# Performance work log

Hardware: AMD Instinct MI355X
Metric: run time of the kernel (lower is better)

The kernel has to match this reference:

```python
import jax, jax.numpy as jnp
import numpy as np

B, Q, MAXK, C, D, H, NL = 64, 16, 32, 64, 768, 512, 2
S = Q * (MAXK + 1) + 1  # max padded sequence length (529)


def lstm_layer(x, w_ih, w_hh, b_ih, b_hh):
    # x: [B, S, Din]; torch gate order i, f, g, o
    xg = jnp.einsum('bsd,gd->bsg', x, w_ih) + b_ih + b_hh  # [B,S,4H]
    h0 = jnp.zeros((x.shape[0], w_hh.shape[1]), x.dtype)

    def step(carry, xt):
        h, c = carry
        g = xt + h @ w_hh.T
        i, f, gg, o = jnp.split(g, 4, axis=-1)
        c = jax.nn.sigmoid(f) * c + jax.nn.sigmoid(i) * jnp.tanh(gg)
        h = jax.nn.sigmoid(o) * jnp.tanh(c)
        return (h, c), h

    _, hs = jax.lax.scan(step, (h0, h0), jnp.swapaxes(xg, 0, 1))
    return jnp.swapaxes(hs, 0, 1)  # [B,S,H]


def build_sequence(text_output, questions_outputs, code_embedding, num_snapshots, que_num):
    # Vectorized equivalent of the nested scatter loops.
    valid_q = jnp.arange(Q)[None, :] < que_num[:, None]          # [B,Q]
    qlen = jnp.where(valid_q, num_snapshots + 1, 0)              # per-question block length
    starts = jnp.cumsum(qlen, axis=1) - qlen                     # exclusive cumsum: block start
    L = jnp.sum(qlen, axis=1)                                    # text position; seq_len = L+1

    buf = jnp.zeros((B, S + 1, D), text_output.dtype)            # extra dump slot at index S
    b1 = jnp.arange(B)[:, None]

    # scatter question embeddings at block starts
    q_dest = jnp.where(valid_q, starts, S)
    buf = buf.at[b1, q_dest].set(questions_outputs)

    # scatter code snapshots: dest = start+1+k, src = code_embedding[b, i+k] (as in source)
    k = jnp.arange(MAXK)
    ns = jnp.where(valid_q, num_snapshots, 0)
    valid_s = k[None, None, :] < ns[:, :, None]                  # [B,Q,K]
    dest = jnp.where(valid_s, starts[:, :, None] + 1 + k[None, None, :], S)
    src = jnp.clip(jnp.arange(Q)[:, None] + k[None, :], 0, C - 1)  # [Q,K]
    code_vals = code_embedding[:, src]                           # [B,Q,K,D]
    buf = buf.at[jnp.arange(B)[:, None, None], dest].set(code_vals)

    # current-question text embedding at end of sequence
    buf = buf.at[jnp.arange(B), L].set(text_output)
    return buf[:, :S], L


def setup_inputs() -> dict:
    key = jax.random.key(0)
    ks = jax.random.split(key, 16)
    inp = {
        'text_output': jax.random.normal(ks[0], (B, D), jnp.float32),
        'questions_outputs': jax.random.normal(ks[1], (B, Q, D), jnp.float32),
        'code_embedding': jax.random.normal(ks[2], (B, C, D), jnp.float32),
        'num_snapshots': jax.random.randint(ks[3], (B, Q), 1, MAXK + 1, jnp.int32),
        'que_num': jax.random.randint(ks[4], (B,), 1, Q + 1, jnp.int32),
    }
    s = 0.02
    inp['w_ih_l0'] = jax.random.normal(ks[5], (4 * H, D), jnp.float32) * s
    inp['w_hh_l0'] = jax.random.normal(ks[6], (4 * H, H), jnp.float32) * s
    inp['b_ih_l0'] = jnp.zeros((4 * H,), jnp.float32)
    inp['b_hh_l0'] = jnp.zeros((4 * H,), jnp.float32)
    inp['w_ih_l1'] = jax.random.normal(ks[7], (4 * H, H), jnp.float32) * s
    inp['w_hh_l1'] = jax.random.normal(ks[8], (4 * H, H), jnp.float32) * s
    inp['b_ih_l1'] = jnp.zeros((4 * H,), jnp.float32)
    inp['b_hh_l1'] = jnp.zeros((4 * H,), jnp.float32)
    inp['fc_w'] = jax.random.normal(ks[9], (1, H), jnp.float32) * s
    inp['fc_b'] = jnp.zeros((1,), jnp.float32)
    return inp


def reference(text_output, questions_outputs, code_embedding, num_snapshots, que_num,
              w_ih_l0, w_hh_l0, b_ih_l0, b_hh_l0,
              w_ih_l1, w_hh_l1, b_ih_l1, b_hh_l1, fc_w, fc_b):
    x, L = build_sequence(text_output, questions_outputs, code_embedding, num_snapshots, que_num)
    h = lstm_layer(x, w_ih_l0, w_hh_l0, b_ih_l0, b_hh_l0)
    h = lstm_layer(h, w_ih_l1, w_hh_l1, b_ih_l1, b_hh_l1)
    last = h[jnp.arange(B), L]  # output at seq_len-1 (= text position)
    return last @ fc_w.T + fc_b  # [B, 1]
```

## Files before the change

### kernel.cpp

```cpp
#include <hip/hip_runtime.h>
#include <hip/hip_cooperative_groups.h>

namespace cg = cooperative_groups;

#define B_    64
#define Q_    16
#define MAXK_ 32
#define C_    64
#define D_    768
#define H_    512
#define G4_   2048
#define S_    529
#define NR_   81

typedef float f32x4_t __attribute__((ext_vector_type(4)));
typedef unsigned int u32x2_t __attribute__((ext_vector_type(2)));
typedef unsigned int u32x4_t __attribute__((ext_vector_type(4)));
typedef _Float16 f16x8_t __attribute__((ext_vector_type(8)));

static constexpr size_t OFF_L     = 0;
static constexpr size_t OFF_MAXL  = 256;
static constexpr size_t OFF_MAP   = 512;
static constexpr size_t OFF_BIAS0 = OFF_MAP   + 135424;
static constexpr size_t OFF_BIAS1 = OFF_BIAS0 + 8192;
static constexpr size_t OFF_C0    = OFF_BIAS1 + 8192;
static constexpr size_t OFF_C1    = OFF_C0    + 131072;
static constexpr size_t OFF_HLAST = OFF_C1    + 131072;
static constexpr size_t OFF_H0B   = OFF_HLAST + 131072;
static constexpr size_t OFF_H1B   = OFF_H0B   + 262144;
static constexpr size_t OFF_WTIH0 = OFF_H1B   + 262144;
static constexpr size_t OFF_XPROJ = OFF_WTIH0 + 6291456ULL;
static constexpr size_t OFF_BAR   = OFF_XPROJ + 42467328ULL;
static constexpr size_t OFF_ORD   = OFF_BAR   + 4096;
static constexpr size_t OFF_GMAX  = OFF_ORD   + 256;
static constexpr size_t WS_NEED   = OFF_GMAX  + 256;

__device__ __forceinline__ int group_base(int g) {
  return (g == 0) ? 0 : (g == 1) ? 16 : (g == 2) ? 48 : 32;
}

__device__ __forceinline__ void store_us_cc(ushort* p, unsigned int v) {
  asm volatile("global_store_short %0, %1, off sc0 sc1" :: "v"(p), "v"(v) : "memory");
}
__device__ __forceinline__ void store_f_cc(float* p, float v) {
  asm volatile("global_store_dword %0, %1, off sc0 sc1" :: "v"(p), "v"(v) : "memory");
}
__device__ __forceinline__ void load_a_cc(u32x4_t& v, const ushort* p) {
  asm volatile("global_load_dwordx4 %0, %1, off sc0 sc1" : "=v"(v) : "v"(p) : "memory");
}

__device__ __forceinline__ unsigned int pkrtz(float a, float b) {
  auto r = __builtin_amdgcn_cvt_pkrtz(a, b);
  unsigned int u;
  __builtin_memcpy(&u, &r, 4);
  return u;
}
__device__ __forceinline__ unsigned int f2h(float a) {
  return pkrtz(a, 0.f) & 0xffffu;
}
__device__ __forceinline__ f32x4_t mfma16(u32x4_t a, u32x4_t b, f32x4_t c) {
  f16x8_t av, bv;
  __builtin_memcpy(&av, &a, 16);
  __builtin_memcpy(&bv, &b, 16);
  return __builtin_amdgcn_mfma_f32_16x16x32_f16(av, bv, c, 0, 0, 0);
}

__device__ __forceinline__ float sigm(float x) { return 1.f/(1.f + __expf(-x)); }

#define PSEG 1280
#define PCOL 20

__global__ __launch_bounds__(256) void k_prep(
    const int* __restrict__ ns, const int* __restrict__ que,
    const float* __restrict__ b_ih0, const float* __restrict__ b_hh0,
    const float* __restrict__ b_ih1, const float* __restrict__ b_hh1,
    int* __restrict__ Lp, int* __restrict__ maxLp, int* __restrict__ map,
    float* __restrict__ bias0, float* __restrict__ bias1,
    float* __restrict__ c0, float* __restrict__ c1, float* __restrict__ hlast,
    ushort* __restrict__ h0b, ushort* __restrict__ h1b, int* __restrict__ bar,
    int* __restrict__ ord, int* __restrict__ gmax)
{
  const int tid = threadIdx.x;
  for (int i = tid; i < B_*S_; i += 256) map[i] = -1;
  for (int i = tid; i < G4_; i += 256) {
    bias0[i] = b_ih0[i] + b_hh0[i];
    bias1[i] = b_ih1[i] + b_hh1[i];
  }
  int* h0i = (int*)h0b;
  int* h1i = (int*)h1b;
  for (int i = tid; i < B_*H_; i += 256) {
    c0[i]=0.f; c1[i]=0.f; hlast[i]=0.f;
    h0i[i]=0; h1i[i]=0;
  }
  for (int i = tid; i < 1024; i += 256) bar[i] = 0;
  if (tid == 0) *maxLp = 0;
  __syncthreads();
  if (tid < B_) {
    const int b = tid;
    const int qn = que[b];
    int pos = 0;
    int* m = map + b*S_;
    for (int q = 0; q < qn; ++q) {
      m[pos++] = q;
      const int n = ns[b*Q_ + q];
      for (int k = 0; k < n; ++k) {
        int j = q + k; if (j > C_-1) j = C_-1;
        m[pos++] = 16 + j;
      }
    }
    m[pos] = 80;
    Lp[b] = pos;
    atomicMax(maxLp, pos);
  }
  __syncthreads();
  if (tid < B_) {
    const int myL = Lp[tid];
    int rank = 0;
    for (int j = 0; j < B_; ++j) {
      const int lj = Lp[j];
      rank += (lj > myL) || (lj == myL && j < tid);
    }
    ord[rank] = tid;
  }
  __syncthreads();
  if (tid < 4) {
    const int gb = (tid == 0) ? 0 : (tid == 1) ? 16 : (tid == 2) ? 48 : 32;
    gmax[tid] = Lp[ord[gb]];
  }
}

__global__ __launch_bounds__(256) void k_transpose(
    const float* __restrict__ w, float* __restrict__ wT)
{
  __shared__ float tile[32][33];
  const int n0 = blockIdx.x * 32;
  const int k0 = blockIdx.y * 32;
  const int tx = threadIdx.x, ty = threadIdx.y;
  for (int i = ty; i < 32; i += 8)
    tile[i][tx] = w[(size_t)(n0+i)*D_ + k0 + tx];
  __syncthreads();
  for (int i = ty; i < 32; i += 8)
    wT[(size_t)(k0 + i)*G4_ + n0 + tx] = tile[tx][i];
}

__global__ __launch_bounds__(128, 2) void k_proj(
    const float* __restrict__ text, const float* __restrict__ ques,
    const float* __restrict__ code, const float* __restrict__ wT_ih0,
    const float* __restrict__ bias0, float* __restrict__ xproj)
{
  __shared__ float hsLds[32][64];
  const int mb = blockIdx.x, nb = blockIdx.y;
  const int n0 = nb * 128;
  const int tid = threadIdx.x;
  const int tb = tid >> 4, tn = tid & 15;
  const int b0 = tb * 8;
  const int bb = tid >> 1, hh = tid & 1;

  const int mrow = mb*64 + bb;
  const int sb = mrow / NR_, sr = mrow % NR_;
  const float* srcrow = (sr < 16) ? (ques + ((size_t)sb*Q_ + sr)*D_)
                      : (sr < 80) ? (code + ((size_t)sb*C_ + (sr-16))*D_)
                                  : (text + (size_t)sb*D_);

  float a[8][8];
  #pragma unroll
  for (int i=0;i<8;i++)
    #pragma unroll
    for (int j=0;j<8;j++) a[i][j]=0.f;

  for (int k0 = 0; k0 < D_; k0 += 32) {
    __syncthreads();
    {
      const float* p = srcrow + k0 + hh*16;
      float4 v0 = *(const float4*)(p+0);
      float4 v1 = *(const float4*)(p+4);
      float4 v2 = *(const float4*)(p+8);
      float4 v3 = *(const float4*)(p+12);
      const int kk = hh*16;
      hsLds[kk+ 0][bb]=v0.x; hsLds[kk+ 1][bb]=v0.y; hsLds[kk+ 2][bb]=v0.z; hsLds[kk+ 3][bb]=v0.w;
      hsLds[kk+ 4][bb]=v1.x; hsLds[kk+ 5][bb]=v1.y; hsLds[kk+ 6][bb]=v1.z; hsLds[kk+ 7][bb]=v1.w;
      hsLds[kk+ 8][bb]=v2.x; hsLds[kk+ 9][bb]=v2.y; hsLds[kk+10][bb]=v2.z; hsLds[kk+11][bb]=v2.w;
      hsLds[kk+12][bb]=v3.x; hsLds[kk+13][bb]=v3.y; hsLds[kk+14][bb]=v3.z; hsLds[kk+15][bb]=v3.w;
    }
    __syncthreads();
    const float* wb = wT_ih0 + (size_t)k0*G4_ + n0 + tn*8;
    #pragma unroll 4
    for (int k=0;k<32;k++){
      float4 w0 = *(const float4*)(wb + (size_t)k*G4_);
      float4 w1 = *(const float4*)(wb + (size_t)k*G4_ + 4);
      float4 hA = *(const float4*)(&hsLds[k][b0]);
      float4 hB = *(const float4*)(&hsLds[k][b0+4]);
      float hv[8]={hA.x,hA.y,hA.z,hA.w,hB.x,hB.y,hB.z,hB.w};
      float wv[8]={w0.x,w0.y,w0.z,w0.w,w1.x,w1.y,w1.z,w1.w};
      #pragma unroll
      for (int i=0;i<8;i++)
        #pragma unroll
        for (int j=0;j<8;j++)
          a[i][j] = fmaf(hv[i], wv[j], a[i][j]);
    }
  }
  float bz[8];
  #pragma unroll
  for (int j=0;j<8;j++) bz[j] = bias0[n0 + tn*8 + j];
  #pragma unroll
  for (int i=0;i<8;i++){
    const int m = mb*64 + b0 + i;
    float* pd = xproj + (size_t)m*G4_ + n0 + tn*8;
    *(float4*)(pd+0) = make_float4(a[i][0]+bz[0], a[i][1]+bz[1], a[i][2]+bz[2], a[i][3]+bz[3]);
    *(float4*)(pd+4) = make_float4(a[i][4]+bz[4], a[i][5]+bz[5], a[i][6]+bz[6], a[i][7]+bz[7]);
  }
}


__device__ __forceinline__ void load_wfrags(int tid, int us,
    const float* __restrict__ w_hh0, const float* __restrict__ w_ih1,
    const float* __restrict__ w_hh1, u32x4_t* wf0, u32x4_t* wf1)
{
  const int wv = tid >> 6, lane = tid & 63;
  const int nidx = lane & 15, kgrp = lane >> 4;
  #pragma unroll
  for (int nt = 0; nt < 4; ++nt) {
    const int ngl = (nidx >> 2)*H_ + us*16 + nt*4 + (nidx & 3);
    const float* r0 = w_hh0 + (size_t)ngl*H_ + wv*128 + kgrp*8;
    #pragma unroll
    for (int f = 0; f < 4; ++f) {
      float4 lo = *(const float4*)(r0 + f*32);
      float4 hi = *(const float4*)(r0 + f*32 + 4);
      wf0[nt*4+f] = (u32x4_t){pkrtz(lo.x,lo.y), pkrtz(lo.z,lo.w), pkrtz(hi.x,hi.y), pkrtz(hi.z,hi.w)};
    }
    const float* w1 = (wv < 2) ? w_ih1 : w_hh1;
    const float* r1 = w1 + (size_t)ngl*H_ + (wv & 1)*256 + kgrp*8;
    #pragma unroll
    for (int f = 0; f < 8; ++f) {
      float4 lo = *(const float4*)(r1 + f*32);
      float4 hi = *(const float4*)(r1 + f*32 + 4);
      wf1[nt*8+f] = (u32x4_t){pkrtz(lo.x,lo.y), pkrtz(lo.z,lo.w), pkrtz(hi.x,hi.y), pkrtz(hi.z,hi.w)};
    }
  }
}

__device__ __forceinline__ void xg_prefetch(int t, int maxLg,
    const int* __restrict__ mrow, const float* __restrict__ xbase,
    float& xg0, float& xg1, float& xg2, float& xg3, int& rpre)
{
  rpre = (t <= maxLg) ? mrow[t] : -1;
  const float* xp = xbase + (size_t)(rpre < 0 ? 0 : rpre)*G4_;
  xg0 = xp[0]; xg1 = xp[512]; xg2 = xp[1024]; xg3 = xp[1536];
}

__device__ __forceinline__ void lstm_iter(int t, int maxLg, int gbase, int us,
    const u32x4_t* wf0, const u32x4_t* wf1, float* __restrict__ P,
    const ushort* __restrict__ h0c, ushort* __restrict__ h0n,
    const ushort* __restrict__ h1c, ushort* __restrict__ h1n,
    float* __restrict__ c0, float* __restrict__ c1, float* __restrict__ hlast,
    const int* __restrict__ mrow, const float* __restrict__ xbase,
    float& xg0, float& xg1, float& xg2, float& xg3, int& rpre0, int& rpre1,
    float b1v0, float b1v1, float b1v2, float b1v3, int Lrb, int rb)
{
  const int tid = threadIdx.x;
  const int wv = tid >> 6, lane = tid & 63;
  const int nidx = lane & 15, kgrp = lane >> 4;

  u32x4_t a0[4], a1[8];
  {
    const ushort* h0r = h0c + (size_t)(gbase + nidx)*H_ + wv*128 + kgrp*8;
    #pragma unroll
    for (int f = 0; f < 4; ++f) load_a_cc(a0[f], h0r + f*32);
    const ushort* hs1 = (wv < 2) ? h0c : h1c;
    const ushort* h1r = hs1 + (size_t)(gbase + nidx)*H_ + (wv & 1)*256 + kgrp*8;
    #pragma unroll
    for (int f = 0; f < 8; ++f) load_a_cc(a1[f], h1r + f*32);
  }
  asm volatile("s_waitcnt vmcnt(0)" ::: "memory");
  __builtin_amdgcn_sched_barrier(0);

  f32x4_t acc0[4], acc1[4];
  #pragma unroll
  for (int nt = 0; nt < 4; ++nt) { acc0[nt] = (f32x4_t){0.f,0.f,0.f,0.f}; acc1[nt] = (f32x4_t){0.f,0.f,0.f,0.f}; }
  #pragma unroll
  for (int nt = 0; nt < 4; ++nt)
    #pragma unroll
    for (int f = 0; f < 4; ++f) acc0[nt] = mfma16(a0[f], wf0[nt*4+f], acc0[nt]);
  #pragma unroll
  for (int nt = 0; nt < 4; ++nt)
    #pragma unroll
    for (int f = 0; f < 8; ++f) acc1[nt] = mfma16(a1[f], wf1[nt*8+f], acc1[nt]);

  #pragma unroll
  for (int nt = 0; nt < 4; ++nt) {
    *(f32x4_t*)(P + (wv*2+0)*PSEG + (nt*16 + nidx)*PCOL + kgrp*4) = acc0[nt];
    *(f32x4_t*)(P + (wv*2+1)*PSEG + (nt*16 + nidx)*PCOL + kgrp*4) = acc1[nt];
  }

  float nxg0=xg0, nxg1=xg1, nxg2=xg2, nxg3=xg3;
  int nr0 = -1;
  const int nr1 = rpre0;
  xg_prefetch(t + 1, maxLg, mrow, xbase, nxg0, nxg1, nxg2, nxg3, nr0);
  __syncthreads();

  const int bl = tid & 15, ul = tid >> 4;
  const int pb = gbase + bl;
  const int u = us*16 + ul;
  const int idx = pb*H_ + u;
  const int clb = (ul >> 2)*16 + (ul & 3);
  if (rpre0 >= 0) {
    float g0=xg0, g1=xg1, g2=xg2, g3=xg3;
    #pragma unroll
    for (int w = 0; w < 4; ++w) {
      const float* Pr = P + (w*2+0)*PSEG + bl;
      g0 += Pr[(clb+ 0)*PCOL]; g1 += Pr[(clb+ 4)*PCOL];
      g2 += Pr[(clb+ 8)*PCOL]; g3 += Pr[(clb+12)*PCOL];
    }
    const float cc = sigm(g1)*c0[idx] + sigm(g0)*tanhf(g2);
    c0[idx] = cc;
    store_us_cc(h0n + idx, f2h(sigm(g3)*tanhf(cc)));
  }
  if (rpre1 >= 0) {
    float g0=b1v0, g1=b1v1, g2=b1v2, g3=b1v3;
    #pragma unroll
    for (int w = 0; w < 4; ++w) {
      const float* Pr = P + (w*2+1)*PSEG + bl;
      g0 += Pr[(clb+ 0)*PCOL]; g1 += Pr[(clb+ 4)*PCOL];
      g2 += Pr[(clb+ 8)*PCOL]; g3 += Pr[(clb+12)*PCOL];
    }
    const float cc = sigm(g1)*c1[idx] + sigm(g0)*tanhf(g2);
    c1[idx] = cc;
    const float hn = sigm(g3)*tanhf(cc);
    store_us_cc(h1n + idx, f2h(hn));
    if (t - 1 == Lrb) store_f_cc(hlast + rb*H_ + u, hn);
  }

  xg0 = nxg0; xg1 = nxg1; xg2 = nxg2; xg3 = nxg3;
  rpre0 = nr0; rpre1 = nr1;
}

__device__ __forceinline__ void grid_barrier_g(int* __restrict__ cnt, int gen)
{
  asm volatile("s_waitcnt vmcnt(0)" ::: "memory");
  __syncthreads();
  if (threadIdx.x == 0) {
    atomicAdd(cnt, 1);
    while (__hip_atomic_load(cnt, __ATOMIC_RELAXED, __HIP_MEMORY_SCOPE_AGENT) < gen*32)
      __builtin_amdgcn_s_sleep(1);
  }
  __syncthreads();
}

__global__ __launch_bounds__(256, 1) void k_lstm_coop(
    const float* __restrict__ w_hh0, const float* __restrict__ w_ih1,
    const float* __restrict__ w_hh1, const float* __restrict__ xproj,
    const float* __restrict__ bias1, const int* __restrict__ Lp,
    const int* __restrict__ gmax, const int* __restrict__ map,
    const int* __restrict__ ord,
    ushort* __restrict__ h0b, ushort* __restrict__ h1b,
    float* __restrict__ c0, float* __restrict__ c1, float* __restrict__ hlast,
    const float* __restrict__ fcw, const float* __restrict__ fcb,
    float* __restrict__ out, int* __restrict__ bar)
{
  __shared__ __align__(16) float P[8*PSEG];
  const int blk = blockIdx.x;
  const int g = blk >> 5, us = blk & 31;
  const int gbase = group_base(g);
  const int tid = threadIdx.x;

  u32x4_t wf0[16], wf1[32];
  load_wfrags(tid, us, w_hh0, w_ih1, w_hh1, wf0, wf1);
  const int maxLg = gmax[g];
  int* cnt = bar + g*64;

  const int rb = ord[gbase + (tid & 15)];
  const int* mrow = map + rb*S_;
  const int u = us*16 + (tid >> 4);
  const float* xbase = xproj + (size_t)rb*NR_*G4_ + u;
  const float b1v0 = bias1[u], b1v1 = bias1[512+u], b1v2 = bias1[1024+u], b1v3 = bias1[1536+u];
  const int Lrb = Lp[rb];

  float xg0=0.f, xg1=0.f, xg2=0.f, xg3=0.f;
  int rpre0 = -1, rpre1 = -1;
  xg_prefetch(0, maxLg, mrow, xbase, xg0, xg1, xg2, xg3, rpre0);
  __syncthreads();

  for (int t = 0; t <= maxLg + 1; ++t) {
    const ushort* h0c = h0b + (size_t)(t & 1)*(B_*H_);
    ushort*       h0n = h0b + (size_t)((t+1) & 1)*(B_*H_);
    const ushort* h1c = h1b + (size_t)(t & 1)*(B_*H_);
    ushort*       h1n = h1b + (size_t)((t+1) & 1)*(B_*H_);
    lstm_iter(t, maxLg, gbase, us, wf0, wf1, P,
              h0c, h0n, h1c, h1n, c0, c1, hlast,
              mrow, xbase, xg0, xg1, xg2, xg3, rpre0, rpre1,
              b1v0, b1v1, b1v2, b1v3, Lrb, rb);
    grid_barrier_g(cnt, t + 1);
  }
  if (us == 0 && tid < 32) {
    const int pb = gbase + (tid >> 1), half = tid & 1;
    const int rbf = ord[pb];
    const float* hv = hlast + (size_t)rbf*H_ + half*256;
    const float* fw = fcw + half*256;
    float s = 0.f;
    #pragma unroll 8
    for (int uu = 0; uu < 256; ++uu) s = fmaf(hv[uu], fw[uu], s);
    s += __shfl_xor(s, 1);
    if (half == 0) store_f_cc(out + rbf, s + fcb[0]);
  }
}

__global__ __launch_bounds__(256, 1) void k_step(int t,
    const float* __restrict__ w_hh0, const float* __restrict__ w_ih1,
    const float* __restrict__ w_hh1, const float* __restrict__ xproj,
    const float* __restrict__ bias1, const int* __restrict__ Lp,
    const int* __restrict__ gmax, const int* __restrict__ map,
    const int* __restrict__ ord,
    ushort* __restrict__ h0b, ushort* __restrict__ h1b,
    float* __restrict__ c0, float* __restrict__ c1, float* __restrict__ hlast)
{
  __shared__ __align__(16) float P[8*PSEG];
  const int blk = blockIdx.x;
  const int g = blk >> 5, us = blk & 31;
  const int gbase = group_base(g);
  const int maxLg = gmax[g];
  if (t > maxLg + 1) return;
  const int tid = threadIdx.x;
  u32x4_t wf0[16], wf1[32];
  load_wfrags(tid, us, w_hh0, w_ih1, w_hh1, wf0, wf1);

  const int rb = ord[gbase + (tid & 15)];
  const int* mrow = map + rb*S_;
  const int u = us*16 + (tid >> 4);
  const float* xbase = xproj + (size_t)rb*NR_*G4_ + u;
  const float b1v0 = bias1[u], b1v1 = bias1[512+u], b1v2 = bias1[1024+u], b1v3 = bias1[1536+u];
  const int Lrb = Lp[rb];

  float xg0=0.f, xg1=0.f, xg2=0.f, xg3=0.f;
  int rpre0 = -1, rpre1 = -1;
  xg_prefetch(t, maxLg, mrow, xbase, xg0, xg1, xg2, xg3, rpre0);
  rpre1 = (t-1 >= 0 && t-1 <= maxLg) ? mrow[t-1] : -1;
  __syncthreads();

  const ushort* h0c = h0b + (size_t)(t & 1)*(B_*H_);
  ushort*       h0n = h0b + (size_t)((t+1) & 1)*(B_*H_);
  const ushort* h1c = h1b + (size_t)(t & 1)*(B_*H_);
  ushort*       h1n = h1b + (size_t)((t+1) & 1)*(B_*H_);
  lstm_iter(t, maxLg, gbase, us, wf0, wf1, P,
            h0c, h0n, h1c, h1n, c0, c1, hlast,
            mrow, xbase, xg0, xg1, xg2, xg3, rpre0, rpre1,
            b1v0, b1v1, b1v2, b1v3, Lrb, rb);
}

__global__ __launch_bounds__(128) void k_fc(
    const float* __restrict__ hlast, const float* __restrict__ fcw,
    const float* __restrict__ fcb, float* __restrict__ out)
{
  const int tid = threadIdx.x;
  if (tid < 128) {
    const int b = tid >> 1, half = tid & 1;
    const float* hv = hlast + (size_t)b*H_ + half*256;
    const float* fw = fcw + half*256;
    float s = 0.f;
    #pragma unroll 8
    for (int u = 0; u < 256; ++u) s = fmaf(hv[u], fw[u], s);
    s += __shfl_xor(s, 1);
    if (half == 0) out[b] = s + fcb[0];
  }
}

extern "C" void kernel_launch(void* const* d_in, const int* in_sizes, int n_in,
                              void* d_out, int out_size, void* d_ws, size_t ws_size,
                              hipStream_t stream)
{
  const float* text  = (const float*)d_in[0];
  const float* ques  = (const float*)d_in[1];
  const float* code  = (const float*)d_in[2];
  const int*   ns    = (const int*)  d_in[3];
  const int*   que   = (const int*)  d_in[4];
  const float* w_ih0 = (const float*)d_in[5];
  const float* w_hh0 = (const float*)d_in[6];
  const float* b_ih0 = (const float*)d_in[7];
  const float* b_hh0 = (const float*)d_in[8];
  const float* w_ih1 = (const float*)d_in[9];
  const float* w_hh1 = (const float*)d_in[10];
  const float* b_ih1 = (const float*)d_in[11];
  const float* b_hh1 = (const float*)d_in[12];
  const float* fcw   = (const float*)d_in[13];
  const float* fcb   = (const float*)d_in[14];
  float* out = (float*)d_out;

  char* ws = (char*)d_ws;
  int*    Lp     = (int*)   (ws + OFF_L);
  int*    maxLp  = (int*)   (ws + OFF_MAXL);
  int*    map    = (int*)   (ws + OFF_MAP);
  float*  bias0  = (float*) (ws + OFF_BIAS0);
  float*  bias1  = (float*) (ws + OFF_BIAS1);
  float*  c0     = (float*) (ws + OFF_C0);
  float*  c1     = (float*) (ws + OFF_C1);
  float*  hlast  = (float*) (ws + OFF_HLAST);
  ushort* h0b    = (ushort*)(ws + OFF_H0B);
  ushort* h1b    = (ushort*)(ws + OFF_H1B);
  float*  wT_ih0 = (float*) (ws + OFF_WTIH0);
  float*  xproj  = (float*) (ws + OFF_XPROJ);
  int*    bar    = (int*)   (ws + OFF_BAR);
  int*    ord    = (int*)   (ws + OFF_ORD);
  int*    gmax   = (int*)   (ws + OFF_GMAX);
  (void)in_sizes; (void)n_in; (void)out_size; (void)ws_size; (void)WS_NEED;

  hipLaunchKernelGGL(k_prep, dim3(1), dim3(256), 0, stream,
                     ns, que, b_ih0, b_hh0, b_ih1, b_hh1,
                     Lp, maxLp, map, bias0, bias1, c0, c1, hlast, h0b, h1b, bar,
                     ord, gmax);

  hipLaunchKernelGGL(k_transpose, dim3(64, 24), dim3(32, 8), 0, stream,
                     w_ih0, wT_ih0);

  hipLaunchKernelGGL(k_proj, dim3(81, 16), dim3(128), 0, stream,
                     text, ques, code, wT_ih0, bias0, xproj);

  const float* a_whh0 = w_hh0; const float* a_wih1 = w_ih1; const float* a_whh1 = w_hh1;
  const float* a_xp = xproj;   const float* a_b1 = bias1;
  const int* a_Lp = Lp; const int* a_gmax = gmax; const int* a_map = map;
  const int* a_ord = ord;
  ushort* a_h0b = h0b; ushort* a_h1b = h1b; float* a_c0 = c0; float* a_c1 = c1;
  float* a_hl = hlast; const float* a_fcw = fcw; const float* a_fcb = fcb;
  float* a_out = out; int* a_bar = bar;
  void* args[] = { &a_whh0, &a_wih1, &a_whh1, &a_xp, &a_b1, &a_Lp, &a_gmax, &a_map,
                   &a_ord, &a_h0b, &a_h1b, &a_c0, &a_c1, &a_hl, &a_fcw, &a_fcb,
                   &a_out, &a_bar };

  hipError_t err = hipLaunchCooperativeKernel((const void*)k_lstm_coop,
                                              dim3(128), dim3(256), args, 0, stream);
  if (err != hipSuccess) {
    (void)hipGetLastError();
    for (int t = 0; t < S_ + 1; ++t) {
      hipLaunchKernelGGL(k_step, dim3(128), dim3(256), 0, stream, t,
                         w_hh0, w_ih1, w_hh1, xproj, bias1, Lp, gmax, map, ord,
                         h0b, h1b, c0, c1, hlast);
    }
    hipLaunchKernelGGL(k_fc, dim3(1), dim3(128), 0, stream, hlast, fcw, fcb, out);
  }
}
```

Baseline: 2.255 ms.

## Replace block-level grid barrier with per-wave counters and use fast tanh

The per-timestep inter-block barrier no longer does __syncthreads plus one polling thread. Each wave now increments its own counter slot (four slots per group), and every wave polls all four slots. This aims to cut the two block-wide syncs and the serialized single-thread spin on the recurrent critical path. It also replaces tanhf with an exp-based approximation in the LSTM cell to shorten the activation math. The risks are correctness of intra-block data visibility (e.g., the shared P buffer, with the __syncthreads now removed from the barrier), more atomic polling traffic, and slightly different tanh accuracy.

Result: slower. 4.201 ms (+86.2%).

```diff
diff --git a/kernel.cpp b/kernel.cpp
--- a/kernel.cpp
+++ b/kernel.cpp
@@ -66,6 +66,9 @@
 }
 
 __device__ __forceinline__ float sigm(float x) { return 1.f/(1.f + __expf(-x)); }
+__device__ __forceinline__ float tanh_fast(float x) {
+  return 1.f - 2.f/(__expf(2.f*x) + 1.f);
+}
 
 #define PSEG 1280
 #define PCOL 20
@@ -211,7 +214,6 @@
   }
 }
 
-
 __device__ __forceinline__ void load_wfrags(int tid, int us,
     const float* __restrict__ w_hh0, const float* __restrict__ w_ih1,
     const float* __restrict__ w_hh1, u32x4_t* wf0, u32x4_t* wf1)
@@ -311,9 +313,9 @@
       g0 += Pr[(clb+ 0)*PCOL]; g1 += Pr[(clb+ 4)*PCOL];
       g2 += Pr[(clb+ 8)*PCOL]; g3 += Pr[(clb+12)*PCOL];
     }
-    const float cc = sigm(g1)*c0[idx] + sigm(g0)*tanhf(g2);
+    const float cc = sigm(g1)*c0[idx] + sigm(g0)*tanh_fast(g2);
     c0[idx] = cc;
-    store_us_cc(h0n + idx, f2h(sigm(g3)*tanhf(cc)));
+    store_us_cc(h0n + idx, f2h(sigm(g3)*tanh_fast(cc)));
   }
   if (rpre1 >= 0) {
     float g0=b1v0, g1=b1v1, g2=b1v2, g3=b1v3;
@@ -323,9 +325,9 @@
       g0 += Pr[(clb+ 0)*PCOL]; g1 += Pr[(clb+ 4)*PCOL];
       g2 += Pr[(clb+ 8)*PCOL]; g3 += Pr[(clb+12)*PCOL];
     }
-    const float cc = sigm(g1)*c1[idx] + sigm(g0)*tanhf(g2);
+    const float cc = sigm(g1)*c1[idx] + sigm(g0)*tanh_fast(g2);
     c1[idx] = cc;
-    const float hn = sigm(g3)*tanhf(cc);
+    const float hn = sigm(g3)*tanh_fast(cc);
     store_us_cc(h1n + idx, f2h(hn));
     if (t - 1 == Lrb) store_f_cc(hlast + rb*H_ + u, hn);
   }
@@ -334,16 +336,21 @@
   rpre0 = nr0; rpre1 = nr1;
 }
 
-__device__ __forceinline__ void grid_barrier_g(int* __restrict__ cnt, int gen)
+__device__ __forceinline__ void wave_barrier_g(int* __restrict__ cnt4, int gen)
 {
   asm volatile("s_waitcnt vmcnt(0)" ::: "memory");
-  __syncthreads();
-  if (threadIdx.x == 0) {
-    atomicAdd(cnt, 1);
-    while (__hip_atomic_load(cnt, __ATOMIC_RELAXED, __HIP_MEMORY_SCOPE_AGENT) < gen*32)
-      __builtin_amdgcn_s_sleep(1);
-  }
-  __syncthreads();
+  const int wv = threadIdx.x >> 6;
+  if ((threadIdx.x & 63) == 0)
+    atomicAdd(cnt4 + wv*16, 1);
+  const int thr = gen*32;
+  for (;;) {
+    const int v0 = __hip_atomic_load(cnt4 +  0, __ATOMIC_RELAXED, __HIP_MEMORY_SCOPE_AGENT);
+    const int v1 = __hip_atomic_load(cnt4 + 16, __ATOMIC_RELAXED, __HIP_MEMORY_SCOPE_AGENT);
+    const int v2 = __hip_atomic_load(cnt4 + 32, __ATOMIC_RELAXED, __HIP_MEMORY_SCOPE_AGENT);
+    const int v3 = __hip_atomic_load(cnt4 + 48, __ATOMIC_RELAXED, __HIP_MEMORY_SCOPE_AGENT);
+    if (v0 >= thr && v1 >= thr && v2 >= thr && v3 >= thr) break;
+    __builtin_amdgcn_s_sleep(1);
+  }
 }
 
 __global__ __launch_bounds__(256, 1) void k_lstm_coop(
@@ -366,7 +373,7 @@
   u32x4_t wf0[16], wf1[32];
   load_wfrags(tid, us, w_hh0, w_ih1, w_hh1, wf0, wf1);
   const int maxLg = gmax[g];
-  int* cnt = bar + g*64;
+  int* cnt4 = bar + g*64;
 
   const int rb = ord[gbase + (tid & 15)];
   const int* mrow = map + rb*S_;
@@ -389,8 +396,9 @@
               h0c, h0n, h1c, h1n, c0, c1, hlast,
               mrow, xbase, xg0, xg1, xg2, xg3, rpre0, rpre1,
               b1v0, b1v1, b1v2, b1v3, Lrb, rb);
-    grid_barrier_g(cnt, t + 1);
-  }
+    wave_barrier_g(cnt4, t + 1);
+  }
+  __syncthreads();
   if (us == 0 && tid < 32) {
     const int pb = gbase + (tid >> 1), half = tid & 1;
     const int rbf = ord[pb];
```
